# Kernel optimization log

Hardware: AMD Instinct MI355X
Metric: run time of the kernel (lower is better)

Reference implementation:

```python
import jax, jax.numpy as jnp
import numpy as np


def setup_inputs() -> dict:
    key = jax.random.key(0)
    k1, k2 = jax.random.split(key)
    B, C, T = 32, 384, 1024
    x = jax.random.normal(k1, (B, C, T), dtype=jnp.float32)
    duration = jax.random.randint(k2, (B, T), 0, 8, dtype=jnp.int32)
    return {"x": x, "duration": duration, "max_len": 7168}


def reference(x, duration, max_len):
    # x: [B, C, T], duration: [B, T] int32
    # Vectorized equivalent of per-phoneme repeat_interleave + pad.
    csum = jnp.cumsum(duration, axis=1)              # [B, T] exclusive-right boundaries
    mel_len = csum[:, -1]                            # [B] total expanded length
    frames = jnp.arange(max_len, dtype=jnp.int32)    # [L]
    # phoneme index owning each output frame: searchsorted skips zero-duration phonemes
    idx = jax.vmap(lambda c: jnp.searchsorted(c, frames, side='right'))(csum)  # [B, L]
    idx = jnp.clip(idx, 0, x.shape[2] - 1)
    out = jnp.take_along_axis(x, idx[:, None, :], axis=2)  # [B, C, L] gather along T
    valid = frames[None, :] < mel_len[:, None]              # [B, L] padding mask
    out = jnp.where(valid[:, None, :], out, jnp.zeros((), dtype=x.dtype))
    return out, mel_len.astype(jnp.int32)
```

## Files before the change

### kernel.cpp

```cpp
#include <hip/hip_runtime.h>


#define B_ 32
#define C_ 384
#define T_ 1024
#define MAXLEN_ 7168
#define FT_ 7
#define CPB_ 8
#define NT_ 256
#define NCG_ (C_ / CPB_)
#define NWG_ (B_ * NCG_)
#define NXCD_ 8

typedef float f32x4 __attribute__((ext_vector_type(4)));

__global__ __launch_bounds__(NT_) void lr_fused_kernel(
    const int* __restrict__ dur,
    const float* __restrict__ x,
    float* __restrict__ out,
    float* __restrict__ mel_out)
{
    const int tid = threadIdx.x;

    const int bid  = blockIdx.x;
    const int wgid = (bid & (NXCD_ - 1)) * (NWG_ / NXCD_) + (bid >> 3);
    const int cblk = wgid % NCG_;
    const int b    = wgid / NCG_;

    __shared__ int s_tok[2][1024];
    __shared__ int s_w[NT_ / 64];

    const int4 d4 = ((const int4*)(dur + b * T_))[tid];
    const int sum4 = d4.x + d4.y + d4.z + d4.w;

    const int lane = tid & 63;
    const int wave = tid >> 6;
    int sc = sum4;
    #pragma unroll
    for (int d = 1; d < 64; d <<= 1) {
        int n = __shfl_up(sc, d, 64);
        if (lane >= d) sc += n;
    }
    if (lane == 63) s_w[wave] = sc;
    __syncthreads();

    int woff = 0;
    #pragma unroll
    for (int w = 0; w < NT_ / 64; ++w)
        woff += (w < wave) ? s_w[w] : 0;
    const int mel = s_w[0] + s_w[1] + s_w[2] + s_w[3];

    if (cblk == 0 && tid == 0)
        mel_out[b] = (float)mel;

    const int st = woff + sc - sum4;
    const int s0 = st;
    const int s1 = s0 + d4.x;
    const int s2 = s1 + d4.y;
    const int s3 = s2 + d4.z;
    const int send = s3 + d4.w;

    const int nvt = (mel + 1023) >> 10;

    const float* xb  = x   + ((size_t)b * C_ + cblk * CPB_) * T_;
    float*       ob0 = out + ((size_t)b * C_ + cblk * CPB_) * MAXLEN_ + (tid << 2);

    for (int ft = 0; ft < nvt; ++ft) {
        int* buf = s_tok[ft & 1];
        const int f0 = ft << 10;

        ((int4*)buf)[tid] = make_int4(-1, -1, -1, -1);
        __syncthreads();

        if (st < f0 + 1024 && send > f0) {
            const int base_tok = tid << 2;
            const int starts[4] = { s0, s1, s2, s3 };
            const int lens[4]   = { d4.x, d4.y, d4.z, d4.w };
            #pragma unroll
            for (int k = 0; k < 4; ++k) {
                int lo = starts[k] - f0;
                int hi = lo + lens[k];
                lo = lo < 0 ? 0 : lo;
                hi = hi > 1024 ? 1024 : hi;
                for (int p = lo; p < hi; ++p)
                    buf[p] = base_tok + k;
            }
        }
        __syncthreads();

        const int4 t4 = ((const int4*)buf)[tid];
        float* ob = ob0 + f0;

        #pragma unroll
        for (int cc = 0; cc < CPB_; ++cc) {
            const float* __restrict__ xr = xb + cc * T_;
            f32x4 v;
            v.x = (t4.x >= 0) ? xr[t4.x] : 0.0f;
            v.y = (t4.y >= 0) ? xr[t4.y] : 0.0f;
            v.z = (t4.z >= 0) ? xr[t4.z] : 0.0f;
            v.w = (t4.w >= 0) ? xr[t4.w] : 0.0f;
            __builtin_nontemporal_store(v, (f32x4*)(ob + (size_t)cc * MAXLEN_));
        }
    }

    const f32x4 z = {0.0f, 0.0f, 0.0f, 0.0f};
    for (int ft = nvt; ft < FT_; ++ft) {
        float* ob = ob0 + (ft << 10);
        #pragma unroll
        for (int cc = 0; cc < CPB_; ++cc)
            __builtin_nontemporal_store(z, (f32x4*)(ob + (size_t)cc * MAXLEN_));
    }
}

extern "C" void kernel_launch(void* const* d_in, const int* in_sizes, int n_in,
                              void* d_out, int out_size, void* d_ws, size_t ws_size,
                              hipStream_t stream) {
    const float* x   = (const float*)d_in[0];
    const int*   dur = (const int*)d_in[1];

    float* out = (float*)d_out;
    float* mel_out = out + (size_t)B_ * C_ * MAXLEN_;

    lr_fused_kernel<<<NWG_, NT_, 0, stream>>>(dur, x, out, mel_out);
}
```

Measured before the change: 74.64 us.

## Build full-length 16-bit token map once and gather all frame tiles unconditionally

```diff
diff --git a/kernel.cpp b/kernel.cpp
--- a/kernel.cpp
+++ b/kernel.cpp
@@ -27,8 +27,17 @@
     const int cblk = wgid % NCG_;
     const int b    = wgid / NCG_;
 
-    __shared__ int s_tok[2][1024];
+    __shared__ unsigned short s_tok[MAXLEN_];
     __shared__ int s_w[NT_ / 64];
+
+    {
+        const int4 f = make_int4(-1, -1, -1, -1);
+        int4* m4 = (int4*)s_tok;
+        m4[tid]       = f;
+        m4[tid + 256] = f;
+        m4[tid + 512] = f;
+        if (tid < 128) m4[tid + 768] = f;
+    }
 
     const int4 d4 = ((const int4*)(dur + b * T_))[tid];
     const int sum4 = d4.x + d4.y + d4.z + d4.w;
@@ -53,62 +62,54 @@
     if (cblk == 0 && tid == 0)
         mel_out[b] = (float)mel;
 
-    const int st = woff + sc - sum4;
-    const int s0 = st;
-    const int s1 = s0 + d4.x;
-    const int s2 = s1 + d4.y;
-    const int s3 = s2 + d4.z;
-    const int send = s3 + d4.w;
+    {
+        const int st = woff + sc - sum4;
+        const int base_tok = tid << 2;
+        const int s0 = st;
+        const int s1 = s0 + d4.x;
+        const int s2 = s1 + d4.y;
+        const int s3 = s2 + d4.z;
+        const int starts[4] = { s0, s1, s2, s3 };
+        const int lens[4]   = { d4.x, d4.y, d4.z, d4.w };
+        #pragma unroll
+        for (int k = 0; k < 4; ++k)
+            for (int p = 0; p < lens[k]; ++p)
+                s_tok[starts[k] + p] = (unsigned short)(base_tok + k);
+    }
+    __syncthreads();
 
-    const int nvt = (mel + 1023) >> 10;
+    unsigned int tk[FT_][2];
+    #pragma unroll
+    for (int ft = 0; ft < FT_; ++ft) {
+        const uint2 u = ((const uint2*)(s_tok + (ft << 10)))[tid];
+        tk[ft][0] = u.x;
+        tk[ft][1] = u.y;
+    }
 
     const float* xb  = x   + ((size_t)b * C_ + cblk * CPB_) * T_;
     float*       ob0 = out + ((size_t)b * C_ + cblk * CPB_) * MAXLEN_ + (tid << 2);
 
-    for (int ft = 0; ft < nvt; ++ft) {
-        int* buf = s_tok[ft & 1];
-        const int f0 = ft << 10;
-
-        ((int4*)buf)[tid] = make_int4(-1, -1, -1, -1);
-        __syncthreads();
-
-        if (st < f0 + 1024 && send > f0) {
-            const int base_tok = tid << 2;
-            const int starts[4] = { s0, s1, s2, s3 };
-            const int lens[4]   = { d4.x, d4.y, d4.z, d4.w };
-            #pragma unroll
-            for (int k = 0; k < 4; ++k) {
-                int lo = starts[k] - f0;
-                int hi = lo + lens[k];
-                lo = lo < 0 ? 0 : lo;
-                hi = hi > 1024 ? 1024 : hi;
-                for (int p = lo; p < hi; ++p)
-                    buf[p] = base_tok + k;
-            }
+    #pragma unroll 2
+    for (int cc = 0; cc < CPB_; ++cc) {
+        const float* __restrict__ xr = xb + cc * T_;
+        float* obc = ob0 + (size_t)cc * MAXLEN_;
+        #pragma unroll
+        for (int ft = 0; ft < FT_; ++ft) {
+            const unsigned int lo = tk[ft][0];
+            const unsigned int hi = tk[ft][1];
+            const unsigned int t0 = lo & 0xFFFFu, t1 = lo >> 16;
+            const unsigned int t2 = hi & 0xFFFFu, t3 = hi >> 16;
+            const float a0 = xr[t0 & 1023u];
+            const float a1 = xr[t1 & 1023u];
+            const float a2 = xr[t2 & 1023u];
+            const float a3 = xr[t3 & 1023u];
+            f32x4 v;
+            v.x = (t0 <= 1023u) ? a0 : 0.0f;
+            v.y = (t1 <= 1023u) ? a1 : 0.0f;
+            v.z = (t2 <= 1023u) ? a2 : 0.0f;
+            v.w = (t3 <= 1023u) ? a3 : 0.0f;
+            __builtin_nontemporal_store(v, (f32x4*)(obc + (ft << 10)));
         }
-        __syncthreads();
-
-        const int4 t4 = ((const int4*)buf)[tid];
-        float* ob = ob0 + f0;
-
-        #pragma unroll
-        for (int cc = 0; cc < CPB_; ++cc) {
-            const float* __restrict__ xr = xb + cc * T_;
-            f32x4 v;
-            v.x = (t4.x >= 0) ? xr[t4.x] : 0.0f;
-            v.y = (t4.y >= 0) ? xr[t4.y] : 0.0f;
-            v.z = (t4.z >= 0) ? xr[t4.z] : 0.0f;
-            v.w = (t4.w >= 0) ? xr[t4.w] : 0.0f;
-            __builtin_nontemporal_store(v, (f32x4*)(ob + (size_t)cc * MAXLEN_));
-        }
-    }
-
-    const f32x4 z = {0.0f, 0.0f, 0.0f, 0.0f};
-    for (int ft = nvt; ft < FT_; ++ft) {
-        float* ob = ob0 + (ft << 10);
-        #pragma unroll
-        for (int cc = 0; cc < CPB_; ++cc)
-            __builtin_nontemporal_store(z, (f32x4*)(ob + (size_t)cc * MAXLEN_));
     }
 }
 
```

Measured after the change: 78.10 us. 1.05x slower.

## Stage x rows in LDS, use 16-bit frame map, halve channels per block

Applied to the files above, without the earlier changes.

```diff
diff --git a/kernel.cpp b/kernel.cpp
--- a/kernel.cpp
+++ b/kernel.cpp
@@ -6,10 +6,10 @@
 #define T_ 1024
 #define MAXLEN_ 7168
 #define FT_ 7
-#define CPB_ 8
+#define CPB_ 4
 #define NT_ 256
 #define NCG_ (C_ / CPB_)
-#define NWG_ (B_ * NCG_)
+#define NWG_ (NCG_ * B_)
 #define NXCD_ 8
 
 typedef float f32x4 __attribute__((ext_vector_type(4)));
@@ -27,7 +27,8 @@
     const int cblk = wgid % NCG_;
     const int b    = wgid / NCG_;
 
-    __shared__ int s_tok[2][1024];
+    __shared__ float s_x[CPB_][T_];
+    __shared__ unsigned short s_map[2][1024];
     __shared__ int s_w[NT_ / 64];
 
     const int4 d4 = ((const int4*)(dur + b * T_))[tid];
@@ -42,6 +43,12 @@
         if (lane >= d) sc += n;
     }
     if (lane == 63) s_w[wave] = sc;
+
+    const float* xb = x + ((size_t)b * C_ + cblk * CPB_) * T_;
+    #pragma unroll
+    for (int r = 0; r < CPB_; ++r)
+        ((f32x4*)s_x[r])[tid] = ((const f32x4*)(xb + r * T_))[tid];
+
     __syncthreads();
 
     int woff = 0;
@@ -62,15 +69,12 @@
 
     const int nvt = (mel + 1023) >> 10;
 
-    const float* xb  = x   + ((size_t)b * C_ + cblk * CPB_) * T_;
-    float*       ob0 = out + ((size_t)b * C_ + cblk * CPB_) * MAXLEN_ + (tid << 2);
+    float* ob0 = out + ((size_t)b * C_ + cblk * CPB_) * MAXLEN_ + (tid << 2);
+    const int fbase = tid << 2;
 
     for (int ft = 0; ft < nvt; ++ft) {
-        int* buf = s_tok[ft & 1];
+        unsigned short* buf = s_map[ft & 1];
         const int f0 = ft << 10;
-
-        ((int4*)buf)[tid] = make_int4(-1, -1, -1, -1);
-        __syncthreads();
 
         if (st < f0 + 1024 && send > f0) {
             const int base_tok = tid << 2;
@@ -83,22 +87,26 @@
                 lo = lo < 0 ? 0 : lo;
                 hi = hi > 1024 ? 1024 : hi;
                 for (int p = lo; p < hi; ++p)
-                    buf[p] = base_tok + k;
+                    buf[p] = (unsigned short)(base_tok + k);
             }
         }
         __syncthreads();
 
-        const int4 t4 = ((const int4*)buf)[tid];
+        const uint2 m = ((const uint2*)buf)[tid];
+        const unsigned int t0 = m.x & 1023u, t1 = (m.x >> 16) & 1023u;
+        const unsigned int t2 = m.y & 1023u, t3 = (m.y >> 16) & 1023u;
+        const int f = f0 + fbase;
+        const bool v0 = (f + 0) < mel, v1 = (f + 1) < mel;
+        const bool v2 = (f + 2) < mel, v3 = (f + 3) < mel;
+
         float* ob = ob0 + f0;
-
         #pragma unroll
         for (int cc = 0; cc < CPB_; ++cc) {
-            const float* __restrict__ xr = xb + cc * T_;
             f32x4 v;
-            v.x = (t4.x >= 0) ? xr[t4.x] : 0.0f;
-            v.y = (t4.y >= 0) ? xr[t4.y] : 0.0f;
-            v.z = (t4.z >= 0) ? xr[t4.z] : 0.0f;
-            v.w = (t4.w >= 0) ? xr[t4.w] : 0.0f;
+            v.x = v0 ? s_x[cc][t0] : 0.0f;
+            v.y = v1 ? s_x[cc][t1] : 0.0f;
+            v.z = v2 ? s_x[cc][t2] : 0.0f;
+            v.w = v3 ? s_x[cc][t3] : 0.0f;
             __builtin_nontemporal_store(v, (f32x4*)(ob + (size_t)cc * MAXLEN_));
         }
     }
```

New measurement: 75.10 us. Within noise of the previous version (+0.6%).
